# Performance work log

Measured on AMD Instinct MI355X. Metric: run time of the kernel, lower is better.

## Reference

```python
import jax, jax.numpy as jnp
import numpy as np

N, K, D, G = 6000, 300, 1024, 16
DG = D // G          # 64 per-head dim
EMB = 64             # position embedding feat_dim


def setup_inputs():
    key = jax.random.key(0)
    ks = jax.random.split(key, 8)
    merged_feat = jax.random.normal(ks[0], (N, D), dtype=jnp.float32)
    u = jax.random.uniform(ks[1], (N, 4), dtype=jnp.float32)
    x1 = u[:, 0] * 800.0
    y1 = u[:, 1] * 800.0
    bboxes = jnp.stack([x1, y1, x1 + u[:, 2] * 200.0 + 8.0, y1 + u[:, 3] * 200.0 + 8.0], axis=1)
    s = 0.02
    Wq = jax.random.normal(ks[2], (D, D), dtype=jnp.float32) * s
    Wk = jax.random.normal(ks[3], (D, D), dtype=jnp.float32) * s
    Wg = jax.random.normal(ks[4], (G, EMB), dtype=jnp.float32) * s
    Wv = jax.random.normal(ks[5], (G, DG, D), dtype=jnp.float32) * s
    bq = jnp.zeros((D,), jnp.float32)
    bk = jnp.zeros((D,), jnp.float32)
    bg = jnp.zeros((G,), jnp.float32)
    bv = jnp.zeros((D,), jnp.float32)
    return dict(merged_feat=merged_feat, bboxes=bboxes, Wq=Wq, bq=bq, Wk=Wk, bk=bk,
                Wg=Wg, bg=bg, Wv=Wv, bv=bv, k=K)


def _cdist(x, y):
    # torch.cdist(p=2): sqrt of clamped squared distances
    sq = jnp.sum(x * x, 1)[:, None] + jnp.sum(y * y, 1)[None, :] - 2.0 * (x @ y.T)
    return jnp.sqrt(jnp.maximum(sq, 0.0))


def _fps_greedy(feat, k):
    # select_farthest_k_sequential: greedy lowest-redundancy sampling on 1/cdist
    Drec = 1.0 / _cdist(feat, feat)  # diagonal -> inf, never argmin-selected

    def step(ds, _):
        idx = jnp.argmin(ds)
        return ds + Drec[idx], idx

    _, rest = jax.lax.scan(step, Drec[0], None, length=k - 1)
    return jnp.concatenate([jnp.zeros((1,), rest.dtype), rest])


def _pos_embedding(bbox, ref_bbox):
    # extract_position_matrix + extract_position_embedding(feat_dim=64)
    xmin, ymin, xmax, ymax = jnp.split(ref_bbox, 4, axis=1)
    wr = xmax - xmin + 1.0
    hr = ymax - ymin + 1.0
    cxr = 0.5 * (xmin + xmax)
    cyr = 0.5 * (ymin + ymax)
    xmin, ymin, xmax, ymax = jnp.split(bbox, 4, axis=1)
    w = xmax - xmin + 1.0
    h = ymax - ymin + 1.0
    cx = 0.5 * (xmin + xmax)
    cy = 0.5 * (ymin + ymax)
    dx = jnp.log(jnp.abs((cx - cxr.T) / w) + 1e-3)
    dy = jnp.log(jnp.abs((cy - cyr.T) / h) + 1e-3)
    dw = jnp.log(w / wr.T)
    dh = jnp.log(h / hr.T)
    pos = jnp.stack([dx, dy, dw, dh], axis=2)            # (k, N, 4)
    rng = jnp.arange(EMB // 8, dtype=jnp.float32)         # 8 frequencies
    dim_mat = jnp.power(1000.0, (8.0 / EMB) * rng)        # (8,)
    div = pos[..., None] * 100.0 / dim_mat               # (k, N, 4, 8)
    emb = jnp.concatenate([jnp.sin(div), jnp.cos(div)], axis=3)  # (k, N, 4, 16)
    return emb.reshape(emb.shape[0], emb.shape[1], EMB)   # (k, N, 64)


def _attention(roi_feat, ref_feat, pos_emb, Wq, bq, Wk, bk, Wg, bg, Wv, bv):
    # attention_module_multi_head: position-gated multi-head relation attention
    k = roi_feat.shape[0]
    # Wgs 1x1 conv (64 -> 16 groups), relu, -> aff_weight (k, G, N)
    aff_weight = jax.nn.relu(jnp.einsum('ge,kne->kgn', Wg, pos_emb) + bg[None, :, None])
    q = (roi_feat @ Wq.T + bq).reshape(k, G, DG)          # (k, G, 64)
    kk = (ref_feat @ Wk.T + bk).reshape(-1, G, DG)        # (N, G, 64)
    aff = jnp.einsum('kgd,ngd->kgn', q, kk) * (1.0 / np.sqrt(float(DG)))
    weighted = jnp.log(aff_weight + 1e-6) + aff
    soft = jax.nn.softmax(weighted, axis=2)               # (k, G, N)
    out_t = jnp.einsum('kgn,nd->kgd', soft, ref_feat)     # (k, G, D)
    # Wvs grouped 1x1 conv (G*D -> D, groups=G)
    return jnp.einsum('kgc,goc->kgo', out_t, Wv).reshape(k, D) + bv


def reference(merged_feat, bboxes, Wq, bq, Wk, bk, Wg, bg, Wv, bv, k):
    idx = _fps_greedy(merged_feat, k)
    roi_feat = merged_feat[idx]
    pos_emb = _pos_embedding(bboxes[idx], bboxes)
    return _attention(roi_feat, merged_feat, pos_emb, Wq, bq, Wk, bk, Wg, bg, Wv, bv)
```

## Files before the change

kernel.cpp:

```cpp
#include <hip/hip_runtime.h>
#include <math.h>

#define N_PTS 6000
#define DIM   1024
#define KSEL  300
#define GG    16
#define DGR   64
#define WSTR  6016
#define XSTR  2048

typedef _Float16 half8 __attribute__((ext_vector_type(8)));
typedef float floatx4 __attribute__((ext_vector_type(4)));

__device__ __forceinline__ unsigned short f2h(float x) {
    _Float16 h = (_Float16)x;
    return __builtin_bit_cast(unsigned short, h);
}
__device__ __forceinline__ float h2f(unsigned short u) {
    return (float)__builtin_bit_cast(_Float16, u);
}

__device__ __forceinline__ void async_copy16(const void* gsrc, void* ldst) {
    __builtin_amdgcn_global_load_lds(
        (const __attribute__((address_space(1))) void*)gsrc,
        (__attribute__((address_space(3))) void*)ldst,
        16, 0, 0);
}

template<bool GRAM, bool OF16>
__global__ __launch_bounds__(256)
void mfma_gemm(const void* Av, long lda, long az,
               const void* Bv, long ldb, long bz,
               void* Cv, long ldc, long cz,
               int M, int N, int Kd,
               const float* __restrict__ bias, long biasz,
               float scale, const float* __restrict__ sqn, int nbm)
{
    __shared__ unsigned short As[128 * 32];
    __shared__ unsigned short Bs[128 * 32];
    const int t = threadIdx.x;
    const int w = t >> 6, l = t & 63;
    const int wr = w >> 1, wc = w & 1;

    int row0, col0, bi = 0, bj = 0;
    if (GRAM) {
        int tt = blockIdx.x, rem = nbm;
        while (tt >= rem) { tt -= rem; bi++; rem--; }
        bj = bi + tt;
        row0 = bi * 128; col0 = bj * 128;
    } else {
        row0 = blockIdx.y * 128; col0 = blockIdx.x * 128;
    }
    const int z = blockIdx.z;
    const unsigned short* Ab = (const unsigned short*)Av + (long)z * az;
    const unsigned short* Bb = (const unsigned short*)Bv + (long)z * bz;

    floatx4 acc[4][4];
#pragma unroll
    for (int i = 0; i < 4; i++)
#pragma unroll
        for (int j = 0; j < 4; j++) acc[i][j] = (floatx4){0.f, 0.f, 0.f, 0.f};

    int ra0 = row0 + (w * 2 + 0) * 16 + (l >> 2); ra0 = ra0 < M ? ra0 : M - 1;
    int ra1 = row0 + (w * 2 + 1) * 16 + (l >> 2); ra1 = ra1 < M ? ra1 : M - 1;
    int rb0 = col0 + (w * 2 + 0) * 16 + (l >> 2); rb0 = rb0 < N ? rb0 : N - 1;
    int rb1 = col0 + (w * 2 + 1) * 16 + (l >> 2); rb1 = rb1 < N ? rb1 : N - 1;
    const long lane_off = (l & 3) * 8;
    const unsigned short* gA0 = Ab + (long)ra0 * lda + lane_off;
    const unsigned short* gA1 = Ab + (long)ra1 * lda + lane_off;
    const unsigned short* gB0 = Bb + (long)rb0 * ldb + lane_off;
    const unsigned short* gB1 = Bb + (long)rb1 * ldb + lane_off;
    unsigned short* lA0 = As + ((w * 2 + 0) * 16) * 32;
    unsigned short* lA1 = As + ((w * 2 + 1) * 16) * 32;
    unsigned short* lB0 = Bs + ((w * 2 + 0) * 16) * 32;
    unsigned short* lB1 = Bs + ((w * 2 + 1) * 16) * 32;

    auto kstep = [&](long offA, long offB) {
        async_copy16(gA0 + offA, (void*)lA0);
        async_copy16(gA1 + offA, (void*)lA1);
        async_copy16(gB0 + offB, (void*)lB0);
        async_copy16(gB1 + offB, (void*)lB1);
        __syncthreads();
        half8 af[4], bfr[4];
#pragma unroll
        for (int ti = 0; ti < 4; ti++)
            af[ti] = *(const half8*)(As + (wr * 64 + ti * 16 + (l & 15)) * 32 + (l >> 4) * 8);
#pragma unroll
        for (int tj = 0; tj < 4; tj++)
            bfr[tj] = *(const half8*)(Bs + (wc * 64 + tj * 16 + (l & 15)) * 32 + (l >> 4) * 8);
#pragma unroll
        for (int ti = 0; ti < 4; ti++)
#pragma unroll
            for (int tj = 0; tj < 4; tj++)
                acc[ti][tj] = __builtin_amdgcn_mfma_f32_16x16x32_f16(
                    af[ti], bfr[tj], acc[ti][tj], 0, 0, 0);
        __syncthreads();
    };

    if (GRAM) {
#pragma unroll 1
        for (int k0 = 0; k0 < 1024; k0 += 32) kstep(k0, k0);
#pragma unroll 1
        for (int k0 = 0; k0 < 1024; k0 += 32) kstep(k0, k0 + 1024);
#pragma unroll 1
        for (int k0 = 0; k0 < 1024; k0 += 32) kstep(k0 + 1024, k0);
    } else {
#pragma unroll 1
        for (int k0 = 0; k0 < Kd; k0 += 32) kstep(k0, k0);
    }

    float* Cf = (float*)Cv + (long)z * cz;
    unsigned short* Ch = (unsigned short*)Cv + (long)z * cz;
    const float* bias_p = bias ? bias + (long)z * biasz : nullptr;
#pragma unroll
    for (int ti = 0; ti < 4; ti++) {
#pragma unroll
        for (int tj = 0; tj < 4; tj++) {
            const int c = col0 + wc * 64 + tj * 16 + (l & 15);
            const int rb = row0 + wr * 64 + ti * 16 + (l >> 4) * 4;
            if (GRAM) {
                float rec4[4];
#pragma unroll
                for (int reg = 0; reg < 4; reg++) {
                    int r = rb + reg;
                    if (r >= M || c >= N) { rec4[reg] = 0.f; continue; }
                    if (r == c) { rec4[reg] = INFINITY; }
                    else {
                        float sq = sqn[r] + sqn[c] - 2.f * acc[ti][tj][reg];
                        rec4[reg] = 1.0f / sqrtf(fmaxf(sq, 0.f));
                    }
                    Cf[(long)r * ldc + c] = rec4[reg];
                }
                if (bi != bj && c < N && rb + 3 < M) {
                    *(float4*)(Cf + (long)c * ldc + rb) =
                        make_float4(rec4[0], rec4[1], rec4[2], rec4[3]);
                }
            } else {
#pragma unroll
                for (int reg = 0; reg < 4; reg++) {
                    int r = rb + reg;
                    if (r >= M || c >= N) continue;
                    float v = acc[ti][tj][reg] * scale;
                    if (bias_p) v += bias_p[c];
                    if (OF16) Ch[(long)r * ldc + c] = f2h(v);
                    else      Cf[(long)r * ldc + c] = v;
                }
            }
        }
    }
}

#define FPS_T 1024

__global__ __launch_bounds__(1024)
void fps_kk_kernel(const float* __restrict__ Drec, int* __restrict__ idxout,
                   const unsigned short* __restrict__ X,
                   const unsigned short* __restrict__ Wk_h,
                   const float* __restrict__ bk,
                   unsigned short* __restrict__ kk_h)
{
    __shared__ unsigned long long red[16];
    __shared__ int s_sel;
    __shared__ unsigned short As[4][128 * 32];
    __shared__ unsigned short Bs[128 * 32];
    const int t = threadIdx.x;

    if (blockIdx.x == 0) {
        const bool act = t < 750;
        float ds[8];
        if (act) {
            const float4* p = (const float4*)Drec + 2 * t;
            float4 a0 = p[0], a1 = p[1];
            ds[0] = a0.x; ds[1] = a0.y; ds[2] = a0.z; ds[3] = a0.w;
            ds[4] = a1.x; ds[5] = a1.y; ds[6] = a1.z; ds[7] = a1.w;
        } else {
#pragma unroll
            for (int j = 0; j < 8; j++) ds[j] = INFINITY;
        }
        if (t == 0) idxout[0] = 0;

        for (int it = 1; it < KSEL; it++) {
            float mv = ds[0]; int mi = 8 * t;
#pragma unroll
            for (int j = 1; j < 8; j++) {
                if (ds[j] < mv) { mv = ds[j]; mi = 8 * t + j; }
            }
            unsigned long long key = act
                ? (((unsigned long long)__float_as_uint(mv) << 32) | (unsigned)mi)
                : ~0ull;
#pragma unroll
            for (int o = 32; o > 0; o >>= 1) {
                unsigned long long other = __shfl_down(key, o);
                if (other < key) key = other;
            }
            if ((t & 63) == 0) red[t >> 6] = key;
            __syncthreads();
            if (t < 64) {
                unsigned long long k2 = (t < 16) ? red[t] : ~0ull;
#pragma unroll
                for (int o = 8; o > 0; o >>= 1) {
                    unsigned long long other = __shfl_down(k2, o);
                    if (other < k2) k2 = other;
                }
                if (t == 0) s_sel = (int)(unsigned)(k2 & 0xffffffffull);
            }
            __syncthreads();
            const int sel = s_sel;
            if (t == 0) idxout[it] = sel;
            if (act) {
                const float4* rp = (const float4*)(Drec + (long)sel * N_PTS) + 2 * t;
                float4 r0 = rp[0], r1 = rp[1];
                ds[0] += r0.x; ds[1] += r0.y; ds[2] += r0.z; ds[3] += r0.w;
                ds[4] += r1.x; ds[5] += r1.y; ds[6] += r1.z; ds[7] += r1.w;
            }
        }
        return;
    }

    const int b = blockIdx.x - 1;
    const int mg = b >> 3;
    const int nt = b & 7;
    const int w = t >> 6, l = t & 63;
    const int sub = w >> 2;
    const int wsu = w & 3;
    const int wr = wsu >> 1, wc = wsu & 1;
    const int row0 = (mg * 4 + sub) * 128;
    const int col0 = nt * 128;

    floatx4 acc[4][4];
#pragma unroll
    for (int i = 0; i < 4; i++)
#pragma unroll
        for (int j = 0; j < 4; j++) acc[i][j] = (floatx4){0.f, 0.f, 0.f, 0.f};

    int ra0 = row0 + (wsu * 2 + 0) * 16 + (l >> 2); ra0 = ra0 < N_PTS ? ra0 : N_PTS - 1;
    int ra1 = row0 + (wsu * 2 + 1) * 16 + (l >> 2); ra1 = ra1 < N_PTS ? ra1 : N_PTS - 1;
    const long lane_off = (l & 3) * 8;
    const unsigned short* gA0 = X + (long)ra0 * XSTR + lane_off;
    const unsigned short* gA1 = X + (long)ra1 * XSTR + lane_off;
    unsigned short* lA0 = As[sub] + ((wsu * 2 + 0) * 16) * 32;
    unsigned short* lA1 = As[sub] + ((wsu * 2 + 1) * 16) * 32;
    const int rb0 = col0 + (wsu * 2 + 0) * 16 + (l >> 2);
    const int rb1 = col0 + (wsu * 2 + 1) * 16 + (l >> 2);
    const unsigned short* gB0 = Wk_h + (long)rb0 * DIM + lane_off;
    const unsigned short* gB1 = Wk_h + (long)rb1 * DIM + lane_off;
    unsigned short* lB0 = Bs + ((wsu * 2 + 0) * 16) * 32;
    unsigned short* lB1 = Bs + ((wsu * 2 + 1) * 16) * 32;

#pragma unroll 1
    for (int k0 = 0; k0 < DIM; k0 += 32) {
        async_copy16(gA0 + k0, (void*)lA0);
        async_copy16(gA1 + k0, (void*)lA1);
        if (sub == 0) {
            async_copy16(gB0 + k0, (void*)lB0);
            async_copy16(gB1 + k0, (void*)lB1);
        }
        __syncthreads();
        half8 af[4], bfr[4];
#pragma unroll
        for (int ti = 0; ti < 4; ti++)
            af[ti] = *(const half8*)(As[sub] + (wr * 64 + ti * 16 + (l & 15)) * 32 + (l >> 4) * 8);
#pragma unroll
        for (int tj = 0; tj < 4; tj++)
            bfr[tj] = *(const half8*)(Bs + (wc * 64 + tj * 16 + (l & 15)) * 32 + (l >> 4) * 8);
#pragma unroll
        for (int ti = 0; ti < 4; ti++)
#pragma unroll
            for (int tj = 0; tj < 4; tj++)
                acc[ti][tj] = __builtin_amdgcn_mfma_f32_16x16x32_f16(
                    af[ti], bfr[tj], acc[ti][tj], 0, 0, 0);
        __syncthreads();
    }

#pragma unroll
    for (int ti = 0; ti < 4; ti++) {
#pragma unroll
        for (int tj = 0; tj < 4; tj++) {
            const int c = col0 + wc * 64 + tj * 16 + (l & 15);
            const int rbase = row0 + wr * 64 + ti * 16 + (l >> 4) * 4;
            const float bkc = bk[c];
#pragma unroll
            for (int reg = 0; reg < 4; reg++) {
                const int r = rbase + reg;
                if (r < N_PTS)
                    kk_h[(long)r * DIM + c] = f2h(acc[ti][tj][reg] + bkc);
            }
        }
    }
}

#define BM 128
#define BN 128
#define BKK 8
#define TM 8
#define TN 8

template<bool TRANSB>
__global__ __launch_bounds__(256)
void sgemm_kernel(const float* __restrict__ A, long lda, long az,
                  const float* __restrict__ B, long ldb, long bz,
                  float* __restrict__ C, long ldc, long cz,
                  int M, int N, int Kd,
                  const float* __restrict__ bias, long biasz, float scale)
{
    __shared__ float As[BKK][BM];
    __shared__ float Bs[BKK][BN];
    const int t = threadIdx.x;
    const int z = blockIdx.z;
    A += (long)z * az; B += (long)z * bz; C += (long)z * cz;
    const float* bias_p = bias ? (bias + (long)z * biasz) : nullptr;
    const int row0 = blockIdx.y * BM;
    const int col0 = blockIdx.x * BN;
    const int tx = t & 15, ty = t >> 4;

    float acc[TM][TN];
#pragma unroll
    for (int i = 0; i < TM; i++)
#pragma unroll
        for (int j = 0; j < TN; j++) acc[i][j] = 0.f;

    const int lrow = t >> 1;
    const int lcol = (t & 1) * 4;

    for (int k0 = 0; k0 < Kd; k0 += BKK) {
        {
            int r = row0 + lrow; r = (r < M) ? r : (M - 1);
            float4 v = *(const float4*)(A + (long)r * lda + (k0 + lcol));
            As[lcol + 0][lrow] = v.x; As[lcol + 1][lrow] = v.y;
            As[lcol + 2][lrow] = v.z; As[lcol + 3][lrow] = v.w;
        }
        {
            int r = col0 + lrow; r = (r < N) ? r : (N - 1);
            float4 v = *(const float4*)(B + (long)r * ldb + (k0 + lcol));
            Bs[lcol + 0][lrow] = v.x; Bs[lcol + 1][lrow] = v.y;
            Bs[lcol + 2][lrow] = v.z; Bs[lcol + 3][lrow] = v.w;
        }
        __syncthreads();
#pragma unroll
        for (int kk = 0; kk < BKK; kk++) {
            float a[TM], b[TN];
#pragma unroll
            for (int i = 0; i < TM; i++) a[i] = As[kk][ty * TM + i];
#pragma unroll
            for (int j = 0; j < TN; j++) b[j] = Bs[kk][tx * TN + j];
#pragma unroll
            for (int i = 0; i < TM; i++)
#pragma unroll
                for (int j = 0; j < TN; j++)
                    acc[i][j] = fmaf(a[i], b[j], acc[i][j]);
        }
        __syncthreads();
    }
#pragma unroll
    for (int i = 0; i < TM; i++) {
        int r = row0 + ty * TM + i;
        if (r >= M) continue;
#pragma unroll
        for (int j = 0; j < TN; j++) {
            int c = col0 + tx * TN + j;
            if (c >= N) continue;
            float v = acc[i][j] * scale;
            if (bias_p) v += bias_p[c];
            C[(long)r * ldc + c] = v;
        }
    }
}

__global__ __launch_bounds__(256)
void sqnpack2_kernel(const float* __restrict__ feat,
                     unsigned short* __restrict__ X, float* __restrict__ sqn)
{
    const int r = blockIdx.x, t = threadIdx.x;
    float4 v = *(const float4*)(feat + (long)r * DIM + t * 4);
    float s = v.x * v.x + v.y * v.y + v.z * v.z + v.w * v.w;

    ushort4 hi, lo;
    hi.x = f2h(v.x); lo.x = f2h(v.x - h2f(hi.x));
    hi.y = f2h(v.y); lo.y = f2h(v.y - h2f(hi.y));
    hi.z = f2h(v.z); lo.z = f2h(v.z - h2f(hi.z));
    hi.w = f2h(v.w); lo.w = f2h(v.w - h2f(hi.w));
    *(ushort4*)(X + (long)r * XSTR + t * 4) = hi;
    *(ushort4*)(X + (long)r * XSTR + 1024 + t * 4) = lo;

#pragma unroll
    for (int o = 32; o > 0; o >>= 1) s += __shfl_down(s, o);
    __shared__ float sr[4];
    if ((t & 63) == 0) sr[t >> 6] = s;
    __syncthreads();
    if (t == 0) sqn[r] = sr[0] + sr[1] + sr[2] + sr[3];
}

__global__ __launch_bounds__(256)
void wconv2_kernel(const float* __restrict__ Wq, const float* __restrict__ Wk,
                   unsigned short* __restrict__ Wq_h, unsigned short* __restrict__ Wk_h)
{
    const int b = blockIdx.x;
    const float* src = (b < 1024) ? Wq : Wk;
    unsigned short* dst = (b < 1024) ? Wq_h : Wk_h;
    const long i = ((long)(b & 1023) * 256 + threadIdx.x) * 4;
    float4 v = *(const float4*)(src + i);
    ushort4 o;
    o.x = f2h(v.x); o.y = f2h(v.y); o.z = f2h(v.z); o.w = f2h(v.w);
    *(ushort4*)(dst + i) = o;
}

__global__ __launch_bounds__(256)
void transpose_kernel(const float* __restrict__ feat, unsigned short* __restrict__ featT)
{
    __shared__ unsigned short tile[32][33];
    const int bx = blockIdx.x;
    const int by = blockIdx.y;
    const int t = threadIdx.x;
    const int lr = t >> 3;
    const int lc = (t & 7) * 4;
    const int r = by * 32 + lr;
    if (r < N_PTS) {
        float4 v = *(const float4*)(feat + (long)r * DIM + bx * 32 + lc);
        tile[lr][lc + 0] = f2h(v.x); tile[lr][lc + 1] = f2h(v.y);
        tile[lr][lc + 2] = f2h(v.z); tile[lr][lc + 3] = f2h(v.w);
    } else {
        tile[lr][lc + 0] = 0; tile[lr][lc + 1] = 0;
        tile[lr][lc + 2] = 0; tile[lr][lc + 3] = 0;
    }
    __syncthreads();
    const int orow = bx * 32 + lr;
    ushort4 o;
    o.x = tile[lc + 0][lr]; o.y = tile[lc + 1][lr];
    o.z = tile[lc + 2][lr]; o.w = tile[lc + 3][lr];
    *(ushort4*)(featT + (long)orow * WSTR + by * 32 + lc) = o;
}

__global__ __launch_bounds__(256)
void gatherb_kernel(const unsigned short* __restrict__ X, const int* __restrict__ idx,
                    unsigned short* __restrict__ roi)
{
    const int k = blockIdx.x, t = threadIdx.x;
    const unsigned short* src = X + (long)idx[k] * XSTR;
    *(ushort4*)(roi + (long)k * DIM + t * 4) = *(const ushort4*)(src + t * 4);
}

__global__ __launch_bounds__(256)
void gatelogit_kernel(const float* __restrict__ bboxes,
                      const int* __restrict__ idx,
                      const float* __restrict__ Wg,
                      const float* __restrict__ bgp,
                      float* __restrict__ W)
{
    __shared__ float swg[GG][64];
    __shared__ float sbg[GG];
    __shared__ float sbb[4];
    const int t = threadIdx.x;
    const int k = blockIdx.y;
    const int n = blockIdx.x * 256 + t;
    for (int i = t; i < GG * 64; i += 256) swg[i >> 6][i & 63] = Wg[i];
    if (t < GG) sbg[t] = bgp[t];
    if (t < 4)  sbb[t] = bboxes[(long)idx[k] * 4 + t];
    __syncthreads();
    if (n >= N_PTS) return;

    const float x1 = sbb[0], y1 = sbb[1], x2 = sbb[2], y2 = sbb[3];
    const float w  = x2 - x1 + 1.f, h = y2 - y1 + 1.f;
    const float cx = 0.5f * (x1 + x2), cy = 0.5f * (y1 + y2);
    float4 rb = *(const float4*)(bboxes + (long)n * 4);
    const float wr = rb.z - rb.x + 1.f, hr = rb.w - rb.y + 1.f;
    const float cxr = 0.5f * (rb.x + rb.z), cyr = 0.5f * (rb.y + rb.w);

    float pos[4];
    pos[0] = __logf(fabsf((cx - cxr) / w) + 1e-3f);
    pos[1] = __logf(fabsf((cy - cyr) / h) + 1e-3f);
    pos[2] = __logf(w / wr);
    pos[3] = __logf(h / hr);

    const float rdm[8] = { 100.0f, 42.169650342858226f, 17.782794100389228f,
                           7.498942093324559f, 3.1622776601683795f,
                           1.333521432163324f, 0.5623413251903491f,
                           0.23713737056616552f };
    float aw[GG];
#pragma unroll
    for (int g = 0; g < GG; g++) aw[g] = sbg[g];
#pragma unroll
    for (int p = 0; p < 4; p++) {
#pragma unroll
        for (int f = 0; f < 8; f++) {
            const float arg = pos[p] * rdm[f];
            const float s_ = __sinf(arg), c_ = __cosf(arg);
            const int e = p * 16 + f;
#pragma unroll
            for (int g = 0; g < GG; g++)
                aw[g] += swg[g][e] * s_ + swg[g][e + 8] * c_;
        }
    }
    float* base = W + ((long)k * GG) * WSTR + n;
#pragma unroll
    for (int g = 0; g < GG; g++) {
        const float lg = __logf(fmaxf(aw[g], 0.f) + 1e-6f);
        base[(long)g * WSTR] += lg;
    }
}

__global__ __launch_bounds__(256)
void softmax16_kernel(float* __restrict__ W)
{
    __shared__ float lg[WSTR];
    __shared__ float sred[4];
    __shared__ float sMS;
    const int t = threadIdx.x;
    float* rowp = W + (long)blockIdx.x * WSTR;

    float m = -INFINITY;
    for (int n = t; n < N_PTS; n += 256) {
        const float v = rowp[n];
        lg[n] = v;
        m = fmaxf(m, v);
    }
#pragma unroll
    for (int o = 32; o > 0; o >>= 1) m = fmaxf(m, __shfl_down(m, o));
    if ((t & 63) == 0) sred[t >> 6] = m;
    __syncthreads();
    if (t == 0) sMS = fmaxf(fmaxf(sred[0], sred[1]), fmaxf(sred[2], sred[3]));
    __syncthreads();
    m = sMS;
    __syncthreads();

    float s = 0.f;
    for (int n = t; n < N_PTS; n += 256) {
        const float e = __expf(lg[n] - m);
        lg[n] = e;
        s += e;
    }
#pragma unroll
    for (int o = 32; o > 0; o >>= 1) s += __shfl_down(s, o);
    if ((t & 63) == 0) sred[t >> 6] = s;
    __syncthreads();
    if (t == 0) sMS = sred[0] + sred[1] + sred[2] + sred[3];
    __syncthreads();
    const float inv = 1.0f / sMS;
    __syncthreads();

    unsigned short* orow = (unsigned short*)rowp;
    for (int n = t; n < WSTR; n += 256)
        orow[n] = (n < N_PTS) ? f2h(lg[n] * inv) : (unsigned short)0;
}

extern "C" void kernel_launch(void* const* d_in, const int* in_sizes, int n_in,
                              void* d_out, int out_size, void* d_ws, size_t ws_size,
                              hipStream_t stream)
{
    const float* feat   = (const float*)d_in[0];
    const float* bboxes = (const float*)d_in[1];
    const float* Wq     = (const float*)d_in[2];
    const float* bq     = (const float*)d_in[3];
    const float* Wk     = (const float*)d_in[4];
    const float* bk     = (const float*)d_in[5];
    const float* Wg     = (const float*)d_in[6];
    const float* bg     = (const float*)d_in[7];
    const float* Wv     = (const float*)d_in[8];
    const float* bv     = (const float*)d_in[9];
    float* out = (float*)d_out;
    float* ws  = (float*)d_ws;

    float* drec = ws;
    float* W    = ws;
    unsigned short* q_h   = (unsigned short*)(ws + 31972000);
    unsigned short* roi_h = (unsigned short*)(ws + 32125600);
    unsigned short* featT = (unsigned short*)(ws + 32300000);
    unsigned short* X     = (unsigned short*)(ws + 36000000);
    float* outt           = ws + 36000000;
    unsigned short* kk_h  = (unsigned short*)(ws + 42144000);
    unsigned short* Wq_h  = (unsigned short*)(ws + 45216000);
    unsigned short* Wk_h  = (unsigned short*)(ws + 45740288);
    float* sqnbuf         = ws + 46264576;
    int*   idxbuf         = (int*)(ws + 46270576);
    if (ws_size < (size_t)185100000) return;

    sqnpack2_kernel<<<N_PTS, 256, 0, stream>>>(feat, X, sqnbuf);
    wconv2_kernel<<<2048, 256, 0, stream>>>(Wq, Wk, Wq_h, Wk_h);

    mfma_gemm<true, false><<<1128, 256, 0, stream>>>(
        X, XSTR, 0, X, XSTR, 0, drec, N_PTS, 0,
        N_PTS, N_PTS, 3072, nullptr, 0, 1.f, sqnbuf, 47);

    fps_kk_kernel<<<97, 1024, 0, stream>>>(drec, idxbuf, X, Wk_h, bk, kk_h);

    transpose_kernel<<<dim3(32, 188), 256, 0, stream>>>(feat, featT);
    gatherb_kernel<<<KSEL, 256, 0, stream>>>(X, idxbuf, roi_h);

    mfma_gemm<false, true><<<dim3(8, 3, 1), 256, 0, stream>>>(
        roi_h, 1024, 0, Wq_h, 1024, 0, q_h, 1024, 0,
        KSEL, DIM, DIM, bq, 0, 1.f, nullptr, 0);

    mfma_gemm<false, false><<<dim3(47, 3, GG), 256, 0, stream>>>(
        q_h, 1024, 64, kk_h, 1024, 64, W, (long)GG * WSTR, WSTR,
        KSEL, N_PTS, 64, nullptr, 0, 0.125f, nullptr, 0);

    gatelogit_kernel<<<dim3(24, KSEL), 256, 0, stream>>>(
        bboxes, idxbuf, Wg, bg, W);
    softmax16_kernel<<<KSEL * GG, 256, 0, stream>>>(W);

    mfma_gemm<false, false><<<dim3(8, 38, 1), 256, 0, stream>>>(
        (unsigned short*)W, 2 * WSTR, 0, featT, WSTR, 0, outt, DIM, 0,
        KSEL * GG, DIM, WSTR, nullptr, 0, 1.f, nullptr, 0);

    sgemm_kernel<true><<<dim3(1, 3, GG), 256, 0, stream>>>(
        outt, (long)GG * DIM, DIM, Wv, DIM, (long)DGR * DIM, out, DIM, DGR,
        KSEL, DGR, DIM, bv, DGR, 1.f);
}
```

Baseline: 1.211 ms.

## Fuse split-precision Gram passes, split-K the attention GEMM, vectorise gate logits

```diff
diff --git a/kernel.cpp b/kernel.cpp
--- a/kernel.cpp
+++ b/kernel.cpp
@@ -27,30 +27,20 @@
         16, 0, 0);
 }
 
-template<bool GRAM, bool OF16>
+template<bool OF16>
 __global__ __launch_bounds__(256)
 void mfma_gemm(const void* Av, long lda, long az,
                const void* Bv, long ldb, long bz,
                void* Cv, long ldc, long cz,
                int M, int N, int Kd,
-               const float* __restrict__ bias, long biasz,
-               float scale, const float* __restrict__ sqn, int nbm)
+               const float* __restrict__ bias, long biasz, float scale)
 {
     __shared__ unsigned short As[128 * 32];
     __shared__ unsigned short Bs[128 * 32];
     const int t = threadIdx.x;
     const int w = t >> 6, l = t & 63;
     const int wr = w >> 1, wc = w & 1;
-
-    int row0, col0, bi = 0, bj = 0;
-    if (GRAM) {
-        int tt = blockIdx.x, rem = nbm;
-        while (tt >= rem) { tt -= rem; bi++; rem--; }
-        bj = bi + tt;
-        row0 = bi * 128; col0 = bj * 128;
-    } else {
-        row0 = blockIdx.y * 128; col0 = blockIdx.x * 128;
-    }
+    const int row0 = blockIdx.y * 128, col0 = blockIdx.x * 128;
     const int z = blockIdx.z;
     const unsigned short* Ab = (const unsigned short*)Av + (long)z * az;
     const unsigned short* Bb = (const unsigned short*)Bv + (long)z * bz;
@@ -75,11 +65,12 @@
     unsigned short* lB0 = Bs + ((w * 2 + 0) * 16) * 32;
     unsigned short* lB1 = Bs + ((w * 2 + 1) * 16) * 32;
 
-    auto kstep = [&](long offA, long offB) {
-        async_copy16(gA0 + offA, (void*)lA0);
-        async_copy16(gA1 + offA, (void*)lA1);
-        async_copy16(gB0 + offB, (void*)lB0);
-        async_copy16(gB1 + offB, (void*)lB1);
+#pragma unroll 1
+    for (int k0 = 0; k0 < Kd; k0 += 32) {
+        async_copy16(gA0 + k0, (void*)lA0);
+        async_copy16(gA1 + k0, (void*)lA1);
+        async_copy16(gB0 + k0, (void*)lB0);
+        async_copy16(gB1 + k0, (void*)lB1);
         __syncthreads();
         half8 af[4], bfr[4];
 #pragma unroll
@@ -95,18 +86,6 @@
                 acc[ti][tj] = __builtin_amdgcn_mfma_f32_16x16x32_f16(
                     af[ti], bfr[tj], acc[ti][tj], 0, 0, 0);
         __syncthreads();
-    };
-
-    if (GRAM) {
-#pragma unroll 1
-        for (int k0 = 0; k0 < 1024; k0 += 32) kstep(k0, k0);
-#pragma unroll 1
-        for (int k0 = 0; k0 < 1024; k0 += 32) kstep(k0, k0 + 1024);
-#pragma unroll 1
-        for (int k0 = 0; k0 < 1024; k0 += 32) kstep(k0 + 1024, k0);
-    } else {
-#pragma unroll 1
-        for (int k0 = 0; k0 < Kd; k0 += 32) kstep(k0, k0);
     }
 
     float* Cf = (float*)Cv + (long)z * cz;
@@ -118,33 +97,119 @@
         for (int tj = 0; tj < 4; tj++) {
             const int c = col0 + wc * 64 + tj * 16 + (l & 15);
             const int rb = row0 + wr * 64 + ti * 16 + (l >> 4) * 4;
-            if (GRAM) {
-                float rec4[4];
-#pragma unroll
-                for (int reg = 0; reg < 4; reg++) {
-                    int r = rb + reg;
-                    if (r >= M || c >= N) { rec4[reg] = 0.f; continue; }
-                    if (r == c) { rec4[reg] = INFINITY; }
-                    else {
-                        float sq = sqn[r] + sqn[c] - 2.f * acc[ti][tj][reg];
-                        rec4[reg] = 1.0f / sqrtf(fmaxf(sq, 0.f));
-                    }
-                    Cf[(long)r * ldc + c] = rec4[reg];
+#pragma unroll
+            for (int reg = 0; reg < 4; reg++) {
+                int r = rb + reg;
+                if (r >= M || c >= N) continue;
+                float v = acc[ti][tj][reg] * scale;
+                if (bias_p) v += bias_p[c];
+                if (OF16) Ch[(long)r * ldc + c] = f2h(v);
+                else      Cf[(long)r * ldc + c] = v;
+            }
+        }
+    }
+}
+
+__global__ __launch_bounds__(256)
+void gram_kernel(const unsigned short* __restrict__ X,
+                 float* __restrict__ C, const float* __restrict__ sqn, int nbm)
+{
+    __shared__ unsigned short Ah[128 * 32], Al[128 * 32];
+    __shared__ unsigned short Bh[128 * 32], Bl[128 * 32];
+    const int t = threadIdx.x;
+    const int w = t >> 6, l = t & 63;
+    const int wr = w >> 1, wc = w & 1;
+
+    int tt = blockIdx.x, rem = nbm, bi = 0;
+    while (tt >= rem) { tt -= rem; bi++; rem--; }
+    const int bj = bi + tt;
+    const int row0 = bi * 128, col0 = bj * 128;
+
+    floatx4 acc[4][4];
+#pragma unroll
+    for (int i = 0; i < 4; i++)
+#pragma unroll
+        for (int j = 0; j < 4; j++) acc[i][j] = (floatx4){0.f, 0.f, 0.f, 0.f};
+
+    int ra0 = row0 + (w * 2 + 0) * 16 + (l >> 2); ra0 = ra0 < N_PTS ? ra0 : N_PTS - 1;
+    int ra1 = row0 + (w * 2 + 1) * 16 + (l >> 2); ra1 = ra1 < N_PTS ? ra1 : N_PTS - 1;
+    int rb0 = col0 + (w * 2 + 0) * 16 + (l >> 2); rb0 = rb0 < N_PTS ? rb0 : N_PTS - 1;
+    int rb1 = col0 + (w * 2 + 1) * 16 + (l >> 2); rb1 = rb1 < N_PTS ? rb1 : N_PTS - 1;
+    const long lane_off = (l & 3) * 8;
+    const unsigned short* gA0 = X + (long)ra0 * XSTR + lane_off;
+    const unsigned short* gA1 = X + (long)ra1 * XSTR + lane_off;
+    const unsigned short* gB0 = X + (long)rb0 * XSTR + lane_off;
+    const unsigned short* gB1 = X + (long)rb1 * XSTR + lane_off;
+    const long ldsoff0 = ((w * 2 + 0) * 16) * 32;
+    const long ldsoff1 = ((w * 2 + 1) * 16) * 32;
+
+#pragma unroll 1
+    for (int k0 = 0; k0 < 1024; k0 += 32) {
+        async_copy16(gA0 + k0, (void*)(Ah + ldsoff0));
+        async_copy16(gA1 + k0, (void*)(Ah + ldsoff1));
+        async_copy16(gA0 + k0 + 1024, (void*)(Al + ldsoff0));
+        async_copy16(gA1 + k0 + 1024, (void*)(Al + ldsoff1));
+        async_copy16(gB0 + k0, (void*)(Bh + ldsoff0));
+        async_copy16(gB1 + k0, (void*)(Bh + ldsoff1));
+        async_copy16(gB0 + k0 + 1024, (void*)(Bl + ldsoff0));
+        async_copy16(gB1 + k0 + 1024, (void*)(Bl + ldsoff1));
+        __syncthreads();
+
+        const long aidx = (wr * 64 + (l & 15)) * 32 + (l >> 4) * 8;
+        const long bidx = (wc * 64 + (l & 15)) * 32 + (l >> 4) * 8;
+        half8 af[4], bfr[4];
+#pragma unroll
+        for (int ti = 0; ti < 4; ti++) af[ti] = *(const half8*)(Ah + aidx + ti * 16 * 32);
+#pragma unroll
+        for (int tj = 0; tj < 4; tj++) bfr[tj] = *(const half8*)(Bh + bidx + tj * 16 * 32);
+#pragma unroll
+        for (int ti = 0; ti < 4; ti++)
+#pragma unroll
+            for (int tj = 0; tj < 4; tj++)
+                acc[ti][tj] = __builtin_amdgcn_mfma_f32_16x16x32_f16(
+                    af[ti], bfr[tj], acc[ti][tj], 0, 0, 0);
+#pragma unroll
+        for (int tj = 0; tj < 4; tj++) bfr[tj] = *(const half8*)(Bl + bidx + tj * 16 * 32);
+#pragma unroll
+        for (int ti = 0; ti < 4; ti++)
+#pragma unroll
+            for (int tj = 0; tj < 4; tj++)
+                acc[ti][tj] = __builtin_amdgcn_mfma_f32_16x16x32_f16(
+                    af[ti], bfr[tj], acc[ti][tj], 0, 0, 0);
+#pragma unroll
+        for (int ti = 0; ti < 4; ti++) af[ti] = *(const half8*)(Al + aidx + ti * 16 * 32);
+#pragma unroll
+        for (int tj = 0; tj < 4; tj++) bfr[tj] = *(const half8*)(Bh + bidx + tj * 16 * 32);
+#pragma unroll
+        for (int ti = 0; ti < 4; ti++)
+#pragma unroll
+            for (int tj = 0; tj < 4; tj++)
+                acc[ti][tj] = __builtin_amdgcn_mfma_f32_16x16x32_f16(
+                    af[ti], bfr[tj], acc[ti][tj], 0, 0, 0);
+        __syncthreads();
+    }
+
+#pragma unroll
+    for (int ti = 0; ti < 4; ti++) {
+#pragma unroll
+        for (int tj = 0; tj < 4; tj++) {
+            const int c = col0 + wc * 64 + tj * 16 + (l & 15);
+            const int rb = row0 + wr * 64 + ti * 16 + (l >> 4) * 4;
+            float rec4[4];
+#pragma unroll
+            for (int reg = 0; reg < 4; reg++) {
+                int r = rb + reg;
+                if (r >= N_PTS || c >= N_PTS) { rec4[reg] = 0.f; continue; }
+                if (r == c) { rec4[reg] = INFINITY; }
+                else {
+                    float sq = sqn[r] + sqn[c] - 2.f * acc[ti][tj][reg];
+                    rec4[reg] = 1.0f / sqrtf(fmaxf(sq, 0.f));
                 }
-                if (bi != bj && c < N && rb + 3 < M) {
-                    *(float4*)(Cf + (long)c * ldc + rb) =
-                        make_float4(rec4[0], rec4[1], rec4[2], rec4[3]);
-                }
-            } else {
-#pragma unroll
-                for (int reg = 0; reg < 4; reg++) {
-                    int r = rb + reg;
-                    if (r >= M || c >= N) continue;
-                    float v = acc[ti][tj][reg] * scale;
-                    if (bias_p) v += bias_p[c];
-                    if (OF16) Ch[(long)r * ldc + c] = f2h(v);
-                    else      Cf[(long)r * ldc + c] = v;
-                }
+                C[(long)r * N_PTS + c] = rec4[reg];
+            }
+            if (bi != bj && c < N_PTS && rb + 3 < N_PTS) {
+                *(float4*)(C + (long)c * N_PTS + rb) =
+                    make_float4(rec4[0], rec4[1], rec4[2], rec4[3]);
             }
         }
     }
@@ -446,13 +511,13 @@
                       const float* __restrict__ bgp,
                       float* __restrict__ W)
 {
-    __shared__ float swg[GG][64];
+    __shared__ float swgT[64][16];
     __shared__ float sbg[GG];
     __shared__ float sbb[4];
     const int t = threadIdx.x;
     const int k = blockIdx.y;
     const int n = blockIdx.x * 256 + t;
-    for (int i = t; i < GG * 64; i += 256) swg[i >> 6][i & 63] = Wg[i];
+    for (int i = t; i < GG * 64; i += 256) swgT[i & 63][i >> 6] = Wg[i];
     if (t < GG) sbg[t] = bgp[t];
     if (t < 4)  sbb[t] = bboxes[(long)idx[k] * 4 + t];
     __syncthreads();
@@ -485,9 +550,16 @@
             const float arg = pos[p] * rdm[f];
             const float s_ = __sinf(arg), c_ = __cosf(arg);
             const int e = p * 16 + f;
-#pragma unroll
-            for (int g = 0; g < GG; g++)
-                aw[g] += swg[g][e] * s_ + swg[g][e + 8] * c_;
+            const float4* s4 = (const float4*)swgT[e];
+            const float4* c4 = (const float4*)swgT[e + 8];
+#pragma unroll
+            for (int gq = 0; gq < 4; gq++) {
+                const float4 sv = s4[gq], cv = c4[gq];
+                aw[gq * 4 + 0] += sv.x * s_ + cv.x * c_;
+                aw[gq * 4 + 1] += sv.y * s_ + cv.y * c_;
+                aw[gq * 4 + 2] += sv.z * s_ + cv.z * c_;
+                aw[gq * 4 + 3] += sv.w * s_ + cv.w * c_;
+            }
         }
     }
     float* base = W + ((long)k * GG) * WSTR + n;
@@ -540,6 +612,16 @@
     unsigned short* orow = (unsigned short*)rowp;
     for (int n = t; n < WSTR; n += 256)
         orow[n] = (n < N_PTS) ? f2h(lg[n] * inv) : (unsigned short)0;
+}
+
+__global__ __launch_bounds__(256)
+void addbuf_kernel(float* __restrict__ a, const float* __restrict__ b)
+{
+    const long i = ((long)blockIdx.x * 256 + threadIdx.x) * 4;
+    float4 va = *(const float4*)(a + i);
+    float4 vb = *(const float4*)(b + i);
+    va.x += vb.x; va.y += vb.y; va.z += vb.z; va.w += vb.w;
+    *(float4*)(a + i) = va;
 }
 
 extern "C" void kernel_launch(void* const* d_in, const int* in_sizes, int n_in,
@@ -561,45 +643,46 @@
 
     float* drec = ws;
     float* W    = ws;
-    unsigned short* q_h   = (unsigned short*)(ws + 31972000);
-    unsigned short* roi_h = (unsigned short*)(ws + 32125600);
-    unsigned short* featT = (unsigned short*)(ws + 32300000);
+    unsigned short* featT = (unsigned short*)(ws + 28900000);
+    float* outt           = ws + 32000000;
+    float* outt2          = ws + 37000000;
     unsigned short* X     = (unsigned short*)(ws + 36000000);
-    float* outt           = ws + 36000000;
-    unsigned short* kk_h  = (unsigned short*)(ws + 42144000);
-    unsigned short* Wq_h  = (unsigned short*)(ws + 45216000);
-    unsigned short* Wk_h  = (unsigned short*)(ws + 45740288);
-    float* sqnbuf         = ws + 46264576;
-    int*   idxbuf         = (int*)(ws + 46270576);
-    if (ws_size < (size_t)185100000) return;
+    unsigned short* kk_h  = (unsigned short*)(ws + 42200000);
+    unsigned short* q_h   = (unsigned short*)(ws + 45280000);
+    unsigned short* roi_h = (unsigned short*)(ws + 45440000);
+    unsigned short* Wq_h  = (unsigned short*)(ws + 45600000);
+    unsigned short* Wk_h  = (unsigned short*)(ws + 46130000);
+    float* sqnbuf         = ws + 46660000;
+    int*   idxbuf         = (int*)(ws + 46666000);
+    if (ws_size < (size_t)186700000) return;
 
     sqnpack2_kernel<<<N_PTS, 256, 0, stream>>>(feat, X, sqnbuf);
     wconv2_kernel<<<2048, 256, 0, stream>>>(Wq, Wk, Wq_h, Wk_h);
 
-    mfma_gemm<true, false><<<1128, 256, 0, stream>>>(
-        X, XSTR, 0, X, XSTR, 0, drec, N_PTS, 0,
-        N_PTS, N_PTS, 3072, nullptr, 0, 1.f, sqnbuf, 47);
+    gram_kernel<<<1128, 256, 0, stream>>>(X, drec, sqnbuf, 47);
 
     fps_kk_kernel<<<97, 1024, 0, stream>>>(drec, idxbuf, X, Wk_h, bk, kk_h);
 
     transpose_kernel<<<dim3(32, 188), 256, 0, stream>>>(feat, featT);
     gatherb_kernel<<<KSEL, 256, 0, stream>>>(X, idxbuf, roi_h);
 
-    mfma_gemm<false, true><<<dim3(8, 3, 1), 256, 0, stream>>>(
+    mfma_gemm<true><<<dim3(8, 3, 1), 256, 0, stream>>>(
         roi_h, 1024, 0, Wq_h, 1024, 0, q_h, 1024, 0,
-        KSEL, DIM, DIM, bq, 0, 1.f, nullptr, 0);
-
-    mfma_gemm<false, false><<<dim3(47, 3, GG), 256, 0, stream>>>(
+        KSEL, DIM, DIM, bq, 0, 1.f);
+
+    mfma_gemm<false><<<dim3(47, 3, GG), 256, 0, stream>>>(
         q_h, 1024, 64, kk_h, 1024, 64, W, (long)GG * WSTR, WSTR,
-        KSEL, N_PTS, 64, nullptr, 0, 0.125f, nullptr, 0);
+        KSEL, N_PTS, 64, nullptr, 0, 0.125f);
 
     gatelogit_kernel<<<dim3(24, KSEL), 256, 0, stream>>>(
         bboxes, idxbuf, Wg, bg, W);
     softmax16_kernel<<<KSEL * GG, 256, 0, stream>>>(W);
 
-    mfma_gemm<false, false><<<dim3(8, 38, 1), 256, 0, stream>>>(
-        (unsigned short*)W, 2 * WSTR, 0, featT, WSTR, 0, outt, DIM, 0,
-        KSEL * GG, DIM, WSTR, nullptr, 0, 1.f, nullptr, 0);
+    mfma_gemm<false><<<dim3(8, 38, 2), 256, 0, stream>>>(
+        (unsigned short*)W, 2 * WSTR, 3008, featT, WSTR, 3008,
+        outt, DIM, 5000000,
+        KSEL * GG, DIM, 3008, nullptr, 0, 1.f);
+    addbuf_kernel<<<4800, 256, 0, stream>>>(outt, outt2);
 
     sgemm_kernel<true><<<dim3(1, 3, GG), 256, 0, stream>>>(
         outt, (long)GG * DIM, DIM, Wv, DIM, (long)DGR * DIM, out, DIM, DGR,
```

Measured after the change: 1.102 ms. 1.1x faster.
